# Optimization experiments

Hardware: AMD Instinct MI355X
Metric: run time of the kernel (lower is better)

The kernel has to match this reference:

```python
import jax, jax.numpy as jnp
import numpy as np

N, E, G = 50000, 800000, 64
DIN, HID, HEADS, L = 128, 128, 4, 3
CH = HID // HEADS  # 32
EPS = 1e-5


def seg_sum(d, ids, n):
    return jax.ops.segment_sum(d, ids, num_segments=n)


def seg_max(d, ids, n):
    return jax.ops.segment_max(d, ids, num_segments=n)


def seg_mean(d, ids, n):
    s = seg_sum(d, ids, n)
    c = seg_sum(jnp.ones((d.shape[0], 1), d.dtype), ids, n)
    return s / jnp.maximum(c, 1.0)


def setup_inputs() -> dict:
    key = jax.random.key(0)
    ks = jax.random.split(key, 24)
    p = lambda k, sh: jax.random.normal(k, sh, jnp.float32) * 0.05
    z = lambda *sh: jnp.zeros(sh, jnp.float32)
    return {
        'x': jax.random.normal(ks[0], (N, DIN), jnp.float32),
        'edge_index': jax.random.randint(ks[1], (2, E), 0, N),
        'batch': jnp.sort(jax.random.randint(ks[2], (N,), 0, G)),
        'proj_W': p(ks[3], (DIN, HID)), 'proj_b': z(HID),
        'gcn_W': p(ks[4], (L, HID, HID)), 'gcn_b': z(L, HID),
        'gat_W': p(ks[5], (L, HID, HID)),
        'gat_asrc': p(ks[6], (L, HEADS, CH)), 'gat_adst': p(ks[7], (L, HEADS, CH)),
        'gat_b': z(L, HID),
        'norm_w': jnp.ones((L, HID), jnp.float32), 'norm_b': z(L, HID),
        'norm_ms': jnp.ones((L, HID), jnp.float32),
        'hub_W1': p(ks[8], (HID, HID // 2)), 'hub_b1': z(HID // 2),
        'hub_W2': p(ks[9], (HID // 2, 4)), 'hub_b2': z(4),
        'att_W1': p(ks[10], (HID, HID // 2)), 'att_b1': z(HID // 2),
        'att_W2': p(ks[11], (HID // 2, 1)), 'att_b2': z(1),
        'pat_W1': p(ks[12], (HID * 2, HID)), 'pat_b1': z(HID),
        'pat_W2': p(ks[13], (HID, HID // 2)), 'pat_b2': z(HID // 2),
        'pat_W3': p(ks[14], (HID // 2, 8)), 'pat_b3': z(8),
        'cls_W1': p(ks[15], (HID + 12, HID)), 'cls_b1': z(HID),
        'cls_W2': p(ks[16], (HID, HID // 2)), 'cls_b2': z(HID // 2),
        'cls_W3': p(ks[17], (HID // 2, 2)), 'cls_b3': z(2),
    }


def _forward(fl, edge_index, batch):
    src, dst = edge_index[0], edge_index[1]
    loops = jnp.arange(N)
    s = jnp.concatenate([src, loops])  # with self-loops (GCN/GAT default)
    d = jnp.concatenate([dst, loops])

    x = fl['x'] @ fl['proj_W'] + fl['proj_b']  # [N, HID]

    # symmetric GCN normalization (shared across layers)
    deg = seg_sum(jnp.ones(s.shape[0], jnp.float32), d, N)
    dis = jnp.where(deg > 0, 1.0 / jnp.sqrt(deg), 0.0)
    coef = (dis[s] * dis[d])[:, None]  # [E+N, 1]

    for i in range(L):
        # GCNConv: out[dst] += norm * (x @ W)[src]
        h_gcn = seg_sum((x @ fl['gcn_W'][i])[s] * coef, d, N) + fl['gcn_b'][i]
        # GATConv (heads=4, concat), eval mode (no dropout)
        hh = (x @ fl['gat_W'][i]).reshape(N, HEADS, CH)
        a_s = (hh * fl['gat_asrc'][i]).sum(-1)  # [N, HEADS]
        a_d = (hh * fl['gat_adst'][i]).sum(-1)
        e = jax.nn.leaky_relu(a_s[s] + a_d[d], negative_slope=0.2)  # [E+N, HEADS]
        e = jnp.exp(e - seg_max(e, d, N)[d])
        alpha = e / seg_sum(e, d, N)[d]
        h_gat = seg_sum(hh[s] * alpha[:, :, None], d, N).reshape(N, HID) + fl['gat_b'][i]
        h = h_gcn + h_gat
        # GraphNorm: per-graph, per-feature
        mean = seg_mean(h, batch, G)
        out = h - fl['norm_ms'][i] * mean[batch]
        var = seg_mean(out * out, batch, G)
        out = out / jnp.sqrt(var[batch] + EPS)
        h = jax.nn.relu(fl['norm_w'][i] * out + fl['norm_b'][i])
        x = h if i == 0 else x + h

    # hub importance: normalized max degree per graph == 1.0 iff any degree > 0
    ones_e = jnp.ones(E, jnp.float32)
    node_deg = seg_sum(ones_e, src, N) + seg_sum(ones_e, dst, N)
    max_deg = seg_max(node_deg, batch, G)
    hub_importance = (max_deg > 0).astype(jnp.float32)

    hub_feat = jax.nn.relu(x @ fl['hub_W1'] + fl['hub_b1']) @ fl['hub_W2'] + fl['hub_b2']
    hub_pooled = seg_mean(hub_feat, batch, G)  # [G, 4]

    # attention pooling: softmax over ALL nodes (dim=0), then per-graph weighted sum
    w = jax.nn.relu(x @ fl['att_W1'] + fl['att_b1']) @ fl['att_W2'] + fl['att_b2']  # [N,1]
    w = jax.nn.softmax(w, axis=0)
    graph_emb = seg_sum(x * w, batch, G)  # [G, HID]

    pattern_emb = jnp.concatenate([seg_mean(x, batch, G), seg_max(x, batch, G)], axis=1)
    pf = jax.nn.relu(pattern_emb @ fl['pat_W1'] + fl['pat_b1'])
    pf = jax.nn.relu(pf @ fl['pat_W2'] + fl['pat_b2'])
    pattern_features = pf @ fl['pat_W3'] + fl['pat_b3']  # [G, 8]

    comb = jnp.concatenate([graph_emb, hub_pooled, pattern_features], axis=1)
    c = jax.nn.relu(comb @ fl['cls_W1'] + fl['cls_b1'])
    c = jax.nn.relu(c @ fl['cls_W2'] + fl['cls_b2'])
    logits = c @ fl['cls_W3'] + fl['cls_b3']  # [G, 2]
    return logits, hub_importance, graph_emb, hub_pooled, pattern_features


def reference(x, edge_index, batch, proj_W, proj_b, gcn_W, gcn_b, gat_W, gat_asrc,
              gat_adst, gat_b, norm_w, norm_b, norm_ms, hub_W1, hub_b1, hub_W2,
              hub_b2, att_W1, att_b1, att_W2, att_b2, pat_W1, pat_b1, pat_W2,
              pat_b2, pat_W3, pat_b3, cls_W1, cls_b1, cls_W2, cls_b2, cls_W3, cls_b3):
    fl = dict(x=x, proj_W=proj_W, proj_b=proj_b, gcn_W=gcn_W, gcn_b=gcn_b,
              gat_W=gat_W, gat_asrc=gat_asrc, gat_adst=gat_adst, gat_b=gat_b,
              norm_w=norm_w, norm_b=norm_b, norm_ms=norm_ms,
              hub_W1=hub_W1, hub_b1=hub_b1, hub_W2=hub_W2, hub_b2=hub_b2,
              att_W1=att_W1, att_b1=att_b1, att_W2=att_W2, att_b2=att_b2,
              pat_W1=pat_W1, pat_b1=pat_b1, pat_W2=pat_W2, pat_b2=pat_b2,
              pat_W3=pat_W3, pat_b3=pat_b3, cls_W1=cls_W1, cls_b1=cls_b1,
              cls_W2=cls_W2, cls_b2=cls_b2, cls_W3=cls_W3, cls_b3=cls_b3)
    return _forward(fl, edge_index, batch)
```

## Files before the change

### kernel.cpp

```cpp
#include <hip/hip_runtime.h>

#define NN 50000
#define NE 800000
#define NG 64
#define HID 128

typedef __attribute__((ext_vector_type(8))) short bf16x8;
typedef __attribute__((ext_vector_type(4))) float f32x4;

__device__ __forceinline__ unsigned short f2b(float f) {
  unsigned u = __float_as_uint(f);
  u += 0x7fffu + ((u >> 16) & 1u);
  return (unsigned short)(u >> 16);
}
__device__ __forceinline__ float b2f(unsigned short b) {
  return __uint_as_float(((unsigned)b) << 16);
}

__global__ void count_edges(const int* __restrict__ ei, int* __restrict__ cnt_dst,
                            int* __restrict__ cnt_src) {
  int e = blockIdx.x * 256 + threadIdx.x;
  if (e >= NE) return;
  atomicAdd(&cnt_src[ei[e]], 1);
  atomicAdd(&cnt_dst[ei[NE + e]], 1);
}

__global__ void scanA_dis(const int* __restrict__ cnt, int* __restrict__ partial,
                          float* __restrict__ dis) {
  __shared__ int s[256];
  int t = threadIdx.x;
  int i = blockIdx.x * 256 + t;
  int v = (i < NN) ? cnt[i] : 0;
  if (i < NN) dis[i] = rsqrtf((float)(v + 1));
  s[t] = v;
  __syncthreads();
  for (int off = 128; off; off >>= 1) {
    if (t < off) s[t] += s[t + off];
    __syncthreads();
  }
  if (!t) partial[blockIdx.x] = s[0];
}

__global__ void scanB_bounds(int* __restrict__ partial, int nb,
                             const int* __restrict__ batch, int* __restrict__ gstart) {
  int t = threadIdx.x;
  if (t == 0) {
    int acc = 0;
    for (int i = 0; i < nb; ++i) { int v = partial[i]; partial[i] = acc; acc += v; }
  }
  if (t >= 1 && t <= NG + 1) {
    int g = t - 1;
    int lo = 0, hi = NN;
    while (lo < hi) { int mid = (lo + hi) >> 1; if (batch[mid] < g) lo = mid + 1; else hi = mid; }
    gstart[g] = lo;
  }
}

__global__ void scanC(const int* __restrict__ cnt, const int* __restrict__ partial,
                      int* __restrict__ rowptr) {
  __shared__ int bufA[256], bufB[256];
  int t = threadIdx.x;
  int i = blockIdx.x * 256 + t;
  int v = (i < NN) ? cnt[i] : 0;
  bufA[t] = v;
  __syncthreads();
  int* src = bufA; int* dst = bufB;
  for (int off = 1; off < 256; off <<= 1) {
    int x = src[t];
    if (t >= off) x += src[t - off];
    dst[t] = x;
    __syncthreads();
    int* tmp = src; src = dst; dst = tmp;
  }
  int incl = src[t];
  if (i < NN) rowptr[i] = partial[blockIdx.x] + incl - v;
  if (i == NN - 1) rowptr[NN] = partial[blockIdx.x] + incl;
}

__global__ void fill_edges(const int* __restrict__ ei, const int* __restrict__ rowptr,
                           int* __restrict__ fillpos, int* __restrict__ col) {
  int e = blockIdx.x * 256 + threadIdx.x;
  if (e >= NE) return;
  int s = ei[e], d = ei[NE + e];
  int p = atomicAdd(&fillpos[d], 1);
  col[rowptr[d] + p] = s;
}

__global__ void prep_all(const float* __restrict__ gcn_W, const float* __restrict__ gat_W,
                         const float* __restrict__ hW1, const float* __restrict__ aW1,
                         const float* __restrict__ projW, unsigned short* __restrict__ wfrag,
                         unsigned short* __restrict__ nfrag, unsigned short* __restrict__ pfrag) {
  int m = blockIdx.y;
  int idx = blockIdx.x * 256 + threadIdx.x;
  int j = idx & 7, lane = (idx >> 3) & 63, t = idx >> 9;
  int ct = t >> 2, ks = t & 3;
  int k = ks * 32 + ((lane >> 4) << 3) + j;
  int c = (ct << 4) + (lane & 15);
  if (m < 3) {
    wfrag[(size_t)m * 32768 + idx] = f2b(gcn_W[(size_t)m * 16384 + k * 128 + c]);
    wfrag[(size_t)m * 32768 + 16384 + idx] = f2b(gat_W[(size_t)m * 16384 + k * 128 + c]);
  } else if (m == 3) {
    float v = (c < 64) ? hW1[k * 64 + c] : aW1[k * 64 + (c - 64)];
    nfrag[idx] = f2b(v);
  } else {
    pfrag[idx] = f2b(projW[k * 128 + c]);
  }
}

__device__ __forceinline__ void load_a_frags_f32(const float* __restrict__ xp, int lane,
                                                 bf16x8 a[4]) {
#pragma unroll
  for (int ks = 0; ks < 4; ++ks) {
    int k0 = ks * 32 + ((lane >> 4) << 3);
    float4 u = *(const float4*)&xp[k0];
    float4 v = *(const float4*)&xp[k0 + 4];
    bf16x8 t;
    t[0] = (short)f2b(u.x); t[1] = (short)f2b(u.y); t[2] = (short)f2b(u.z); t[3] = (short)f2b(u.w);
    t[4] = (short)f2b(v.x); t[5] = (short)f2b(v.y); t[6] = (short)f2b(v.z); t[7] = (short)f2b(v.w);
    a[ks] = t;
  }
}

__device__ __forceinline__ void load_a_frags_b16(const unsigned short* __restrict__ xp,
                                                 int lane, bf16x8 a[4]) {
#pragma unroll
  for (int ks = 0; ks < 4; ++ks) {
    int k0 = ks * 32 + ((lane >> 4) << 3);
    a[ks] = *(const bf16x8*)&xp[k0];
  }
}

__global__ __launch_bounds__(256) void gemm_proj_mfma(
    const float* __restrict__ X, const unsigned short* __restrict__ F,
    const float* __restrict__ bias, float* __restrict__ Y,
    unsigned short* __restrict__ YB, int nrows) {
  __shared__ float Ys[64 * 128];
  int tid = threadIdx.x;
  int w = tid >> 6, lane = tid & 63;
  int row0 = blockIdx.x * 64;
  int row = row0 + w * 16 + (lane & 15);
  const float* xp = (row < nrows) ? &X[(size_t)row * 128] : &X[0];
  bf16x8 a[4];
  load_a_frags_f32(xp, lane, a);
  f32x4 acc[8];
#pragma unroll
  for (int ct = 0; ct < 8; ++ct) acc[ct] = (f32x4){0.f, 0.f, 0.f, 0.f};
#pragma unroll
  for (int ct = 0; ct < 8; ++ct) {
#pragma unroll
    for (int ks = 0; ks < 4; ++ks) {
      bf16x8 b = *(const bf16x8*)&F[((ct * 4 + ks) * 64 + lane) * 8];
      acc[ct] = __builtin_amdgcn_mfma_f32_16x16x32_bf16(a[ks], b, acc[ct], 0, 0, 0);
    }
  }
#pragma unroll
  for (int ct = 0; ct < 8; ++ct) {
    int c = (ct << 4) + (lane & 15);
    float bv = bias[c];
#pragma unroll
    for (int j = 0; j < 4; ++j) {
      int r = w * 16 + ((lane >> 4) << 2) + j;
      Ys[r * 128 + c] = acc[ct][j] + bv;
    }
  }
  __syncthreads();
  int nr = min(nrows - row0, 64);
  const float4* ys4 = (const float4*)Ys;
  float4* y4 = (float4*)(Y + (size_t)row0 * 128);
  ushort4* yb4 = (ushort4*)(YB + (size_t)row0 * 128);
  for (int e = tid; e < nr * 32; e += 256) {
    float4 v = ys4[e];
    y4[e] = v;
    ushort4 b;
    b.x = f2b(v.x); b.y = f2b(v.y); b.z = f2b(v.z); b.w = f2b(v.w);
    yb4[e] = b;
  }
}

__global__ __launch_bounds__(256) void gemm_dual_mfma(
    const unsigned short* __restrict__ XB, const unsigned short* __restrict__ F1,
    const unsigned short* __restrict__ F2, const float* __restrict__ asrc,
    const float* __restrict__ adst, const float* __restrict__ dis,
    unsigned short* __restrict__ G, float* __restrict__ a_s, float* __restrict__ a_d,
    int nrows) {
  __shared__ unsigned short Gs[64 * 256];
  int tid = threadIdx.x;
  int w = tid >> 6, lane = tid & 63;
  int row0 = blockIdx.x * 64;
  int row = row0 + w * 16 + (lane & 15);
  const unsigned short* xp = (row < nrows) ? &XB[(size_t)row * 128] : &XB[0];
  bf16x8 a[4];
  load_a_frags_b16(xp, lane, a);
  f32x4 acc1[8], acc2[8];
#pragma unroll
  for (int ct = 0; ct < 8; ++ct) {
    acc1[ct] = (f32x4){0.f, 0.f, 0.f, 0.f};
    acc2[ct] = (f32x4){0.f, 0.f, 0.f, 0.f};
  }
#pragma unroll
  for (int ct = 0; ct < 8; ++ct) {
#pragma unroll
    for (int ks = 0; ks < 4; ++ks) {
      int off = ((ct * 4 + ks) * 64 + lane) * 8;
      bf16x8 b1 = *(const bf16x8*)&F1[off];
      bf16x8 b2 = *(const bf16x8*)&F2[off];
      acc1[ct] = __builtin_amdgcn_mfma_f32_16x16x32_bf16(a[ks], b1, acc1[ct], 0, 0, 0);
      acc2[ct] = __builtin_amdgcn_mfma_f32_16x16x32_bf16(a[ks], b2, acc2[ct], 0, 0, 0);
    }
  }
  float dv[4];
#pragma unroll
  for (int j = 0; j < 4; ++j) {
    int gr = row0 + w * 16 + ((lane >> 4) << 2) + j;
    dv[j] = dis[gr < nrows ? gr : 0];
  }
#pragma unroll
  for (int ct = 0; ct < 8; ++ct) {
#pragma unroll
    for (int j = 0; j < 4; ++j) {
      int r = w * 16 + ((lane >> 4) << 2) + j;
      int c = (ct << 4) + (lane & 15);
      Gs[r * 256 + c] = f2b(acc1[ct][j] * dv[j]);
      Gs[r * 256 + 128 + c] = f2b(acc2[ct][j]);
    }
  }
  __syncthreads();
  int nr = min(nrows - row0, 64);
  const uint4* gs4 = (const uint4*)Gs;
  uint4* g4 = (uint4*)(G + (size_t)row0 * 256);
  for (int e = tid; e < nr * 32; e += 256) g4[e] = gs4[e];
  int f = 2 * lane;
  float as0 = asrc[f], as1 = asrc[f + 1];
  float ad0 = adst[f], ad1 = adst[f + 1];
  for (int i = 0; i < 16; ++i) {
    int r = w * 16 + i;
    int n = row0 + r;
    if (n >= nrows) break;
    ushort2 v = *(const ushort2*)&Gs[r * 256 + 128 + f];
    float x0 = b2f(v.x), x1 = b2f(v.y);
    float ps = x0 * as0 + x1 * as1;
    float pd = x0 * ad0 + x1 * ad1;
    ps += __shfl_xor(ps, 1); pd += __shfl_xor(pd, 1);
    ps += __shfl_xor(ps, 2); pd += __shfl_xor(pd, 2);
    ps += __shfl_xor(ps, 4); pd += __shfl_xor(pd, 4);
    ps += __shfl_xor(ps, 8); pd += __shfl_xor(pd, 8);
    if ((lane & 15) == 0) {
      int h = lane >> 4;
      a_s[n * 4 + h] = ps;
      a_d[n * 4 + h] = pd;
    }
  }
}

__global__ __launch_bounds__(256) void node_mlps_mfma(
    const unsigned short* __restrict__ XB, const unsigned short* __restrict__ Fn,
    const float* __restrict__ hb1, const float* __restrict__ ab1,
    const float* __restrict__ hW2, const float* __restrict__ hb2,
    const float* __restrict__ aW2, const float* __restrict__ ab2,
    float* __restrict__ hub_feat, float* __restrict__ w_att) {
  __shared__ float Hs[64 * 133];
  int tid = threadIdx.x;
  int w = tid >> 6, lane = tid & 63;
  int row0 = blockIdx.x * 64;
  int row = row0 + w * 16 + (lane & 15);
  const unsigned short* xp = (row < NN) ? &XB[(size_t)row * 128] : &XB[0];
  bf16x8 a[4];
  load_a_frags_b16(xp, lane, a);
  f32x4 acc[8];
#pragma unroll
  for (int ct = 0; ct < 8; ++ct) acc[ct] = (f32x4){0.f, 0.f, 0.f, 0.f};
#pragma unroll
  for (int ct = 0; ct < 8; ++ct) {
#pragma unroll
    for (int ks = 0; ks < 4; ++ks) {
      bf16x8 b = *(const bf16x8*)&Fn[((ct * 4 + ks) * 64 + lane) * 8];
      acc[ct] = __builtin_amdgcn_mfma_f32_16x16x32_bf16(a[ks], b, acc[ct], 0, 0, 0);
    }
  }
#pragma unroll
  for (int ct = 0; ct < 8; ++ct) {
    int c = (ct << 4) + (lane & 15);
    float bias = (c < 64) ? hb1[c] : ab1[c - 64];
#pragma unroll
    for (int j = 0; j < 4; ++j) {
      int r = w * 16 + ((lane >> 4) << 2) + j;
      float v = acc[ct][j] + bias;
      Hs[r * 133 + c] = v > 0.f ? v : 0.f;
    }
  }
  __syncthreads();
  int r = tid & 63, o = tid >> 6;
  int n = row0 + r;
  if (n < NN) {
    float d = hb2[o];
#pragma unroll 8
    for (int k = 0; k < 64; ++k) d += Hs[r * 133 + k] * hW2[k * 4 + o];
    hub_feat[n * 4 + o] = d;
    if (tid < 64) {
      float d2 = ab2[0];
#pragma unroll 8
      for (int k = 0; k < 64; ++k) d2 += Hs[r * 133 + 64 + k] * aW2[k];
      w_att[n] = d2;
    }
  }
}

__device__ __forceinline__ float lrelu(float v) { return v > 0.f ? v : 0.2f * v; }

__global__ __launch_bounds__(256) void edge_aggregate_p(
    const unsigned short* __restrict__ G, const float* __restrict__ a_s,
    const float* __restrict__ a_d, const float* __restrict__ dis,
    const int* __restrict__ rowptr, const int* __restrict__ col,
    const float* __restrict__ gcn_b, const float* __restrict__ gat_b,
    float* __restrict__ hout, float* __restrict__ S1z) {
  if (blockIdx.x == 0) {
    for (int i = threadIdx.x; i < 2 * NG * 128; i += 256) S1z[i] = 0.f;
  }
  int n = blockIdx.x * 4 + (threadIdx.x >> 6);
  int lane = threadIdx.x & 63;
  int es = lane >> 4, fl = lane & 15;
  int h = fl >> 2;
  int f8 = fl << 3;
  int p0 = rowptr[n], p1 = rowptr[n + 1];
  int cnt = p1 - p0 + 1;
  float adh = a_d[n * 4 + h];
  float dn = dis[n];
  float ag[8] = {0.f, 0.f, 0.f, 0.f, 0.f, 0.f, 0.f, 0.f};
  float aa[8] = {0.f, 0.f, 0.f, 0.f, 0.f, 0.f, 0.f, 0.f};
  float ssum = 0.f;
#define EDGE_ACC(eu, xv, hv)                                \
  do {                                                      \
    ag[0] += __uint_as_float((xv).x << 16);                 \
    ag[1] += __uint_as_float((xv).x & 0xffff0000u);         \
    ag[2] += __uint_as_float((xv).y << 16);                 \
    ag[3] += __uint_as_float((xv).y & 0xffff0000u);         \
    ag[4] += __uint_as_float((xv).z << 16);                 \
    ag[5] += __uint_as_float((xv).z & 0xffff0000u);         \
    ag[6] += __uint_as_float((xv).w << 16);                 \
    ag[7] += __uint_as_float((xv).w & 0xffff0000u);         \
    aa[0] += (eu)*__uint_as_float((hv).x << 16);            \
    aa[1] += (eu)*__uint_as_float((hv).x & 0xffff0000u);    \
    aa[2] += (eu)*__uint_as_float((hv).y << 16);            \
    aa[3] += (eu)*__uint_as_float((hv).y & 0xffff0000u);    \
    aa[4] += (eu)*__uint_as_float((hv).z << 16);            \
    aa[5] += (eu)*__uint_as_float((hv).z & 0xffff0000u);    \
    aa[6] += (eu)*__uint_as_float((hv).w << 16);            \
    aa[7] += (eu)*__uint_as_float((hv).w & 0xffff0000u);    \
  } while (0)
  int e = es;
  for (; e + 4 < cnt; e += 8) {
    int eB = e + 4;
    int srcA = (e < cnt - 1) ? col[p0 + e] : n;
    int srcB = (eB < cnt - 1) ? col[p0 + eB] : n;
    float euA = __expf(lrelu(a_s[srcA * 4 + h] + adh));
    float euB = __expf(lrelu(a_s[srcB * 4 + h] + adh));
    uint4 xvA = *(const uint4*)&G[(size_t)srcA * 256 + f8];
    uint4 hvA = *(const uint4*)&G[(size_t)srcA * 256 + 128 + f8];
    uint4 xvB = *(const uint4*)&G[(size_t)srcB * 256 + f8];
    uint4 hvB = *(const uint4*)&G[(size_t)srcB * 256 + 128 + f8];
    ssum += euA + euB;
    EDGE_ACC(euA, xvA, hvA);
    EDGE_ACC(euB, xvB, hvB);
  }
  for (; e < cnt; e += 4) {
    int src = (e < cnt - 1) ? col[p0 + e] : n;
    float eu = __expf(lrelu(a_s[src * 4 + h] + adh));
    uint4 xv = *(const uint4*)&G[(size_t)src * 256 + f8];
    uint4 hv = *(const uint4*)&G[(size_t)src * 256 + 128 + f8];
    ssum += eu;
    EDGE_ACC(eu, xv, hv);
  }
#undef EDGE_ACC
#pragma unroll
  for (int j = 0; j < 8; ++j) {
    ag[j] += __shfl_xor(ag[j], 16); ag[j] += __shfl_xor(ag[j], 32);
    aa[j] += __shfl_xor(aa[j], 16); aa[j] += __shfl_xor(aa[j], 32);
  }
  ssum += __shfl_xor(ssum, 16); ssum += __shfl_xor(ssum, 32);
  if (es == 0) {
    float rs = 1.f / ssum;
    float4 gb0 = *(const float4*)&gcn_b[f8];
    float4 gb1 = *(const float4*)&gcn_b[f8 + 4];
    float4 tb0 = *(const float4*)&gat_b[f8];
    float4 tb1 = *(const float4*)&gat_b[f8 + 4];
    float4 o0, o1;
    o0.x = ag[0] * dn + aa[0] * rs + gb0.x + tb0.x;
    o0.y = ag[1] * dn + aa[1] * rs + gb0.y + tb0.y;
    o0.z = ag[2] * dn + aa[2] * rs + gb0.z + tb0.z;
    o0.w = ag[3] * dn + aa[3] * rs + gb0.w + tb0.w;
    o1.x = ag[4] * dn + aa[4] * rs + gb1.x + tb1.x;
    o1.y = ag[5] * dn + aa[5] * rs + gb1.y + tb1.y;
    o1.z = ag[6] * dn + aa[6] * rs + gb1.z + tb1.z;
    o1.w = ag[7] * dn + aa[7] * rs + gb1.w + tb1.w;
    *(float4*)&hout[n * 128 + f8] = o0;
    *(float4*)&hout[n * 128 + f8 + 4] = o1;
  }
}

__global__ __launch_bounds__(128) void graph_stats_par(
    const float* __restrict__ h, const int* __restrict__ batch,
    float* __restrict__ S1, float* __restrict__ S2) {
  int f = threadIdx.x;
  int n0 = blockIdx.x * 64;
  int n1 = min(n0 + 64, NN);
  int g = batch[n0];
  float s1 = 0.f, s2 = 0.f;
  for (int n = n0; n < n1; ++n) {
    int gn = batch[n];
    if (gn != g) {
      atomicAdd(&S1[g * 128 + f], s1);
      atomicAdd(&S2[g * 128 + f], s2);
      s1 = 0.f; s2 = 0.f; g = gn;
    }
    float v = h[n * 128 + f];
    s1 += v; s2 += v * v;
  }
  atomicAdd(&S1[g * 128 + f], s1);
  atomicAdd(&S2[g * 128 + f], s2);
}

__global__ __launch_bounds__(256) void graph_norm(
    const float* __restrict__ h, const int* __restrict__ batch,
    const int* __restrict__ gstart, const float* __restrict__ S1,
    const float* __restrict__ S2, const float* __restrict__ nw,
    const float* __restrict__ nb, const float* __restrict__ nms,
    float* __restrict__ x, unsigned short* __restrict__ xb, int layer) {
  int idx = blockIdx.x * 256 + threadIdx.x;
  if (idx >= NN * 32) return;
  int n = idx >> 5, fq = (idx & 31) << 2;
  int g = batch[n];
  float c = fmaxf((float)(gstart[g + 1] - gstart[g]), 1.f);
  float rc = 1.f / c;
  float4 s1 = *(const float4*)&S1[g * 128 + fq];
  float4 s2 = *(const float4*)&S2[g * 128 + fq];
  float4 ms = *(const float4*)&nms[fq];
  float4 w = *(const float4*)&nw[fq];
  float4 b = *(const float4*)&nb[fq];
  float4 hv = *(const float4*)&h[(size_t)n * 128 + fq];
  float4 o;
#define GN1(X)                                                           \
  {                                                                      \
    float mean = s1.X * rc;                                              \
    float var = s2.X * rc - mean * mean * ms.X * (2.f - ms.X);           \
    var = fmaxf(var, 0.f);                                               \
    float ot = (hv.X - ms.X * mean) * rsqrtf(var + 1e-5f);               \
    float t = w.X * ot + b.X;                                            \
    o.X = t > 0.f ? t : 0.f;                                             \
  }
  GN1(x) GN1(y) GN1(z) GN1(w)
#undef GN1
  float4* xp = (float4*)&x[(size_t)n * 128 + fq];
  float4 xo;
  if (layer == 0) {
    xo = o;
  } else {
    xo = *xp;
    xo.x += o.x; xo.y += o.y; xo.z += o.z; xo.w += o.w;
  }
  *xp = xo;
  ushort4 bo;
  bo.x = f2b(xo.x); bo.y = f2b(xo.y); bo.z = f2b(xo.z); bo.w = f2b(xo.w);
  *(ushort4*)&xb[(size_t)n * 128 + fq] = bo;
}

__global__ void reduce_sum1(const float* __restrict__ w, float* __restrict__ tmpS,
                            float* __restrict__ poolZ, int zcount) {
  __shared__ float s[256];
  int t = threadIdx.x;
  if (blockIdx.x == 0) {
    for (int i = t; i < zcount; i += 256) poolZ[i] = 0.f;
  }
  float acc = 0.f;
  for (int i = blockIdx.x * 256 + t; i < NN; i += gridDim.x * 256) acc += __expf(w[i]);
  s[t] = acc;
  __syncthreads();
  for (int off = 128; off; off >>= 1) {
    if (t < off) s[t] += s[t + off];
    __syncthreads();
  }
  if (!t) tmpS[blockIdx.x] = s[0];
}

__global__ void reduce_sum2(const float* __restrict__ tmpS, float* __restrict__ scal) {
  __shared__ float s[256];
  int t = threadIdx.x;
  s[t] = tmpS[t];
  __syncthreads();
  for (int off = 128; off; off >>= 1) {
    if (t < off) s[t] += s[t + off];
    __syncthreads();
  }
  if (!t) scal[1] = s[0];
}

__global__ __launch_bounds__(128) void graph_pool_par(
    const float* __restrict__ x, const float* __restrict__ hub_feat,
    const float* __restrict__ w_att, const int* __restrict__ batch,
    float* __restrict__ Sx, unsigned* __restrict__ Mx, float* __restrict__ WSx,
    float* __restrict__ Shub) {
  int f = threadIdx.x;
  int n0 = blockIdx.x * 64;
  int n1 = min(n0 + 64, NN);
  int g = batch[n0];
  float sx = 0.f, wx = 0.f, mx = 0.f, sh = 0.f;
  for (int n = n0; n < n1; ++n) {
    int gn = batch[n];
    if (gn != g) {
      atomicAdd(&Sx[g * 128 + f], sx);
      atomicAdd(&WSx[g * 128 + f], wx);
      atomicMax(&Mx[g * 128 + f], __float_as_uint(mx));
      if (f < 4) atomicAdd(&Shub[g * 4 + f], sh);
      sx = 0.f; wx = 0.f; mx = 0.f; sh = 0.f; g = gn;
    }
    float xv = x[n * 128 + f];
    float ew = __expf(w_att[n]);
    sx += xv;
    wx += ew * xv;
    mx = fmaxf(mx, xv);
    if (f < 4) sh += hub_feat[n * 4 + f];
  }
  atomicAdd(&Sx[g * 128 + f], sx);
  atomicAdd(&WSx[g * 128 + f], wx);
  atomicMax(&Mx[g * 128 + f], __float_as_uint(mx));
  if (f < 4) atomicAdd(&Shub[g * 4 + f], sh);
}

__global__ __launch_bounds__(128) void finalize(
    const float* __restrict__ Sx, const float* __restrict__ Mx,
    const float* __restrict__ WSx, const float* __restrict__ Shub,
    const float* __restrict__ scal, const int* __restrict__ gstart,
    const int* __restrict__ cnt_src, const int* __restrict__ cnt_dst,
    const float* __restrict__ pW1, const float* __restrict__ pb1,
    const float* __restrict__ pW2, const float* __restrict__ pb2,
    const float* __restrict__ pW3, const float* __restrict__ pb3,
    const float* __restrict__ cW1, const float* __restrict__ cb1,
    const float* __restrict__ cW2, const float* __restrict__ cb2,
    const float* __restrict__ cW3, const float* __restrict__ cb3,
    float* __restrict__ out) {
  int g = blockIdx.x, t = threadIdx.x;
  __shared__ float pe[256], comb[140], buf1[128], buf2[64];
  __shared__ int snd[128];
  int s = gstart[g], e = gstart[g + 1];
  float c = fmaxf((float)(e - s), 1.f);
  int mdeg = 0;
  for (int n = s + t; n < e; n += 128) mdeg = max(mdeg, cnt_src[n] + cnt_dst[n]);
  snd[t] = mdeg;
  float* out_logits = out;
  float* out_hub = out + 128;
  float* out_ge = out + 192;
  float* out_hp = out + 192 + 8192;
  float* out_pf = out + 192 + 8192 + 256;
  float ge = WSx[g * 128 + t] / scal[1];
  out_ge[g * 128 + t] = ge;
  comb[t] = ge;
  pe[t] = Sx[g * 128 + t] / c;
  pe[128 + t] = Mx[g * 128 + t];
  if (t < 4) {
    float hp = Shub[g * 4 + t] / c;
    out_hp[g * 4 + t] = hp;
    comb[128 + t] = hp;
  }
  __syncthreads();
  for (int off = 64; off; off >>= 1) {
    if (t < off) snd[t] = max(snd[t], snd[t + off]);
    __syncthreads();
  }
  if (t == 0) out_hub[g] = (snd[0] > 0) ? 1.f : 0.f;
  float v = pb1[t];
  for (int k = 0; k < 256; ++k) v += pe[k] * pW1[k * 128 + t];
  buf1[t] = v > 0.f ? v : 0.f;
  __syncthreads();
  if (t < 64) {
    float v2 = pb2[t];
    for (int k = 0; k < 128; ++k) v2 += buf1[k] * pW2[k * 64 + t];
    buf2[t] = v2 > 0.f ? v2 : 0.f;
  }
  __syncthreads();
  if (t < 8) {
    float v3 = pb3[t];
    for (int k = 0; k < 64; ++k) v3 += buf2[k] * pW3[k * 8 + t];
    out_pf[g * 8 + t] = v3;
    comb[132 + t] = v3;
  }
  __syncthreads();
  float u = cb1[t];
  for (int k = 0; k < 140; ++k) u += comb[k] * cW1[k * 128 + t];
  buf1[t] = u > 0.f ? u : 0.f;
  __syncthreads();
  if (t < 64) {
    float u2 = cb2[t];
    for (int k = 0; k < 128; ++k) u2 += buf1[k] * cW2[k * 64 + t];
    buf2[t] = u2 > 0.f ? u2 : 0.f;
  }
  __syncthreads();
  if (t < 2) {
    float u3 = cb3[t];
    for (int k = 0; k < 64; ++k) u3 += buf2[k] * cW3[k * 2 + t];
    out_logits[g * 2 + t] = u3;
  }
}

extern "C" void kernel_launch(void* const* d_in, const int* in_sizes, int n_in,
                              void* d_out, int out_size, void* d_ws, size_t ws_size,
                              hipStream_t stream) {
  const float* x_in = (const float*)d_in[0];
  const int* ei = (const int*)d_in[1];
  const int* batch = (const int*)d_in[2];
  const float* proj_W = (const float*)d_in[3];
  const float* proj_b = (const float*)d_in[4];
  const float* gcn_W = (const float*)d_in[5];
  const float* gcn_b = (const float*)d_in[6];
  const float* gat_W = (const float*)d_in[7];
  const float* gat_as = (const float*)d_in[8];
  const float* gat_ad = (const float*)d_in[9];
  const float* gat_b = (const float*)d_in[10];
  const float* norm_w = (const float*)d_in[11];
  const float* norm_b = (const float*)d_in[12];
  const float* norm_ms = (const float*)d_in[13];
  const float* hub_W1 = (const float*)d_in[14];
  const float* hub_b1 = (const float*)d_in[15];
  const float* hub_W2 = (const float*)d_in[16];
  const float* hub_b2 = (const float*)d_in[17];
  const float* att_W1 = (const float*)d_in[18];
  const float* att_b1 = (const float*)d_in[19];
  const float* att_W2 = (const float*)d_in[20];
  const float* att_b2 = (const float*)d_in[21];
  const float* pat_W1 = (const float*)d_in[22];
  const float* pat_b1 = (const float*)d_in[23];
  const float* pat_W2 = (const float*)d_in[24];
  const float* pat_b2 = (const float*)d_in[25];
  const float* pat_W3 = (const float*)d_in[26];
  const float* pat_b3 = (const float*)d_in[27];
  const float* cls_W1 = (const float*)d_in[28];
  const float* cls_b1 = (const float*)d_in[29];
  const float* cls_W2 = (const float*)d_in[30];
  const float* cls_b2 = (const float*)d_in[31];
  const float* cls_W3 = (const float*)d_in[32];
  const float* cls_b3 = (const float*)d_in[33];
  float* out = (float*)d_out;

  char* ws = (char*)d_ws;
  auto fbuf = [&](size_t n) { float* p = (float*)ws; ws += ((n * 4 + 255) / 256) * 256; return p; };
  auto ibuf = [&](size_t n) { int* p = (int*)ws; ws += ((n * 4 + 255) / 256) * 256; return p; };

  float* x = fbuf((size_t)NN * 128);
  unsigned short* xb = (unsigned short*)fbuf((size_t)NN * 64);
  unsigned short* gath = (unsigned short*)fbuf((size_t)NN * 128);
  float* h = fbuf((size_t)NN * 128);
  unsigned short* wfrag = (unsigned short*)fbuf(3 * 32768 / 2);
  unsigned short* nfrag = (unsigned short*)fbuf(16384 / 2);
  unsigned short* pfrag = (unsigned short*)fbuf(16384 / 2);
  float* a_s = fbuf((size_t)NN * 4);
  float* a_d = fbuf((size_t)NN * 4);
  float* dis = fbuf(NN);
  float* w_att = fbuf(NN);
  float* hub_feat = fbuf((size_t)NN * 4);
  float* S1 = fbuf(NG * 128);
  float* S2 = fbuf(NG * 128);
  float* Sx = fbuf(NG * 128);
  float* Mx = fbuf(NG * 128);
  float* WSx = fbuf(NG * 128);
  float* Shub = fbuf(NG * 4);
  float* tmpS = fbuf(256);
  float* scal = fbuf(4);
  int* zero0 = ibuf(3 * NN);
  int* cnt_dst = zero0;
  int* cnt_src = zero0 + NN;
  int* fillpos = zero0 + 2 * NN;
  int* rowptr = ibuf(NN + 1);
  int* col = ibuf(NE);
  int* partial = ibuf(256);
  int* gstart = ibuf(NG + 1);

  const int NB = (NN + 255) / 256;
  const int NC = (NN + 63) / 64;
  const int GM = (NN + 63) / 64;

  hipMemsetAsync(zero0, 0, (size_t)3 * NN * 4, stream);
  count_edges<<<NE / 256, 256, 0, stream>>>(ei, cnt_dst, cnt_src);
  scanA_dis<<<NB, 256, 0, stream>>>(cnt_dst, partial, dis);
  scanB_bounds<<<1, 128, 0, stream>>>(partial, NB, batch, gstart);
  scanC<<<NB, 256, 0, stream>>>(cnt_dst, partial, rowptr);
  fill_edges<<<NE / 256, 256, 0, stream>>>(ei, rowptr, fillpos, col);
  prep_all<<<dim3(64, 5), 256, 0, stream>>>(gcn_W, gat_W, hub_W1, att_W1, proj_W,
                                            wfrag, nfrag, pfrag);

  gemm_proj_mfma<<<GM, 256, 0, stream>>>(x_in, pfrag, proj_b, x, xb, NN);

  for (int l = 0; l < 3; ++l) {
    gemm_dual_mfma<<<GM, 256, 0, stream>>>(xb, wfrag + (size_t)l * 32768,
                                           wfrag + (size_t)l * 32768 + 16384,
                                           gat_as + l * 128, gat_ad + l * 128, dis,
                                           gath, a_s, a_d, NN);
    edge_aggregate_p<<<NN / 4, 256, 0, stream>>>(gath, a_s, a_d, dis, rowptr, col,
                                                 gcn_b + l * 128, gat_b + l * 128, h, S1);
    graph_stats_par<<<NC, 128, 0, stream>>>(h, batch, S1, S2);
    graph_norm<<<(NN * 32 + 255) / 256, 256, 0, stream>>>(h, batch, gstart, S1, S2,
                                                          norm_w + l * 128, norm_b + l * 128,
                                                          norm_ms + l * 128, x, xb, l);
  }

  node_mlps_mfma<<<GM, 256, 0, stream>>>(xb, nfrag, hub_b1, att_b1, hub_W2, hub_b2,
                                         att_W2, att_b2, hub_feat, w_att);

  reduce_sum1<<<256, 256, 0, stream>>>(w_att, tmpS, Sx, 3 * NG * 128 + NG * 4);
  reduce_sum2<<<1, 256, 0, stream>>>(tmpS, scal);

  graph_pool_par<<<NC, 128, 0, stream>>>(x, hub_feat, w_att, batch,
                                         Sx, (unsigned*)Mx, WSx, Shub);

  finalize<<<NG, 128, 0, stream>>>(Sx, Mx, WSx, Shub, scal, gstart, cnt_src, cnt_dst,
                                   pat_W1, pat_b1, pat_W2, pat_b2, pat_W3, pat_b3,
                                   cls_W1, cls_b1, cls_W2, cls_b2, cls_W3, cls_b3, out);
}
```

Measured before the change: 598.5 us.

## Drop fp32 residual stream, fuse graph stats into aggregation and pooling into MLP

Keeps the residual node features only in bf16, so the fp32 x buffer and its reads and writes go away. Per-graph sum and sum-of-squares statistics are accumulated inside the edge aggregation kernel, with LDS pre-reduction when all four nodes in a block share a graph, which removes the separate stats pass over h. Node MLPs and graph pooling are merged into one kernel, and the two-stage exp-sum reduction becomes a single atomic pass. Zeroing of accumulators moves into the memset and the dual GEMM. The residual stream now accumulates in bf16, which adds rounding error across layers.

```diff
diff --git a/kernel.cpp b/kernel.cpp
--- a/kernel.cpp
+++ b/kernel.cpp
@@ -132,9 +132,8 @@
 
 __global__ __launch_bounds__(256) void gemm_proj_mfma(
     const float* __restrict__ X, const unsigned short* __restrict__ F,
-    const float* __restrict__ bias, float* __restrict__ Y,
-    unsigned short* __restrict__ YB, int nrows) {
-  __shared__ float Ys[64 * 128];
+    const float* __restrict__ bias, unsigned short* __restrict__ XB, int nrows) {
+  __shared__ unsigned short Ys[64 * 128];
   int tid = threadIdx.x;
   int w = tid >> 6, lane = tid & 63;
   int row0 = blockIdx.x * 64;
@@ -160,21 +159,14 @@
 #pragma unroll
     for (int j = 0; j < 4; ++j) {
       int r = w * 16 + ((lane >> 4) << 2) + j;
-      Ys[r * 128 + c] = acc[ct][j] + bv;
+      Ys[r * 128 + c] = f2b(acc[ct][j] + bv);
     }
   }
   __syncthreads();
   int nr = min(nrows - row0, 64);
-  const float4* ys4 = (const float4*)Ys;
-  float4* y4 = (float4*)(Y + (size_t)row0 * 128);
-  ushort4* yb4 = (ushort4*)(YB + (size_t)row0 * 128);
-  for (int e = tid; e < nr * 32; e += 256) {
-    float4 v = ys4[e];
-    y4[e] = v;
-    ushort4 b;
-    b.x = f2b(v.x); b.y = f2b(v.y); b.z = f2b(v.z); b.w = f2b(v.w);
-    yb4[e] = b;
-  }
+  const uint4* ys4 = (const uint4*)Ys;
+  uint4* y4 = (uint4*)(XB + (size_t)row0 * 128);
+  for (int e = tid; e < nr * 16; e += 256) y4[e] = ys4[e];
 }
 
 __global__ __launch_bounds__(256) void gemm_dual_mfma(
@@ -182,7 +174,10 @@
     const unsigned short* __restrict__ F2, const float* __restrict__ asrc,
     const float* __restrict__ adst, const float* __restrict__ dis,
     unsigned short* __restrict__ G, float* __restrict__ a_s, float* __restrict__ a_d,
-    int nrows) {
+    float* __restrict__ S1z, int nrows) {
+  if (blockIdx.x == 0) {
+    for (int i = threadIdx.x; i < 2 * NG * 128; i += 256) S1z[i] = 0.f;
+  }
   __shared__ unsigned short Gs[64 * 256];
   int tid = threadIdx.x;
   int w = tid >> 6, lane = tid & 63;
@@ -252,72 +247,20 @@
   }
 }
 
-__global__ __launch_bounds__(256) void node_mlps_mfma(
-    const unsigned short* __restrict__ XB, const unsigned short* __restrict__ Fn,
-    const float* __restrict__ hb1, const float* __restrict__ ab1,
-    const float* __restrict__ hW2, const float* __restrict__ hb2,
-    const float* __restrict__ aW2, const float* __restrict__ ab2,
-    float* __restrict__ hub_feat, float* __restrict__ w_att) {
-  __shared__ float Hs[64 * 133];
-  int tid = threadIdx.x;
-  int w = tid >> 6, lane = tid & 63;
-  int row0 = blockIdx.x * 64;
-  int row = row0 + w * 16 + (lane & 15);
-  const unsigned short* xp = (row < NN) ? &XB[(size_t)row * 128] : &XB[0];
-  bf16x8 a[4];
-  load_a_frags_b16(xp, lane, a);
-  f32x4 acc[8];
-#pragma unroll
-  for (int ct = 0; ct < 8; ++ct) acc[ct] = (f32x4){0.f, 0.f, 0.f, 0.f};
-#pragma unroll
-  for (int ct = 0; ct < 8; ++ct) {
-#pragma unroll
-    for (int ks = 0; ks < 4; ++ks) {
-      bf16x8 b = *(const bf16x8*)&Fn[((ct * 4 + ks) * 64 + lane) * 8];
-      acc[ct] = __builtin_amdgcn_mfma_f32_16x16x32_bf16(a[ks], b, acc[ct], 0, 0, 0);
-    }
-  }
-#pragma unroll
-  for (int ct = 0; ct < 8; ++ct) {
-    int c = (ct << 4) + (lane & 15);
-    float bias = (c < 64) ? hb1[c] : ab1[c - 64];
-#pragma unroll
-    for (int j = 0; j < 4; ++j) {
-      int r = w * 16 + ((lane >> 4) << 2) + j;
-      float v = acc[ct][j] + bias;
-      Hs[r * 133 + c] = v > 0.f ? v : 0.f;
-    }
-  }
-  __syncthreads();
-  int r = tid & 63, o = tid >> 6;
-  int n = row0 + r;
-  if (n < NN) {
-    float d = hb2[o];
-#pragma unroll 8
-    for (int k = 0; k < 64; ++k) d += Hs[r * 133 + k] * hW2[k * 4 + o];
-    hub_feat[n * 4 + o] = d;
-    if (tid < 64) {
-      float d2 = ab2[0];
-#pragma unroll 8
-      for (int k = 0; k < 64; ++k) d2 += Hs[r * 133 + 64 + k] * aW2[k];
-      w_att[n] = d2;
-    }
-  }
-}
-
 __device__ __forceinline__ float lrelu(float v) { return v > 0.f ? v : 0.2f * v; }
 
 __global__ __launch_bounds__(256) void edge_aggregate_p(
     const unsigned short* __restrict__ G, const float* __restrict__ a_s,
     const float* __restrict__ a_d, const float* __restrict__ dis,
     const int* __restrict__ rowptr, const int* __restrict__ col,
-    const float* __restrict__ gcn_b, const float* __restrict__ gat_b,
-    float* __restrict__ hout, float* __restrict__ S1z) {
-  if (blockIdx.x == 0) {
-    for (int i = threadIdx.x; i < 2 * NG * 128; i += 256) S1z[i] = 0.f;
-  }
-  int n = blockIdx.x * 4 + (threadIdx.x >> 6);
-  int lane = threadIdx.x & 63;
+    const int* __restrict__ batch, const float* __restrict__ gcn_b,
+    const float* __restrict__ gat_b, float* __restrict__ hout,
+    float* __restrict__ S1, float* __restrict__ S2) {
+  __shared__ float S1loc[128], S2loc[128];
+  int tid = threadIdx.x;
+  if (tid < 128) { S1loc[tid] = 0.f; S2loc[tid] = 0.f; }
+  int n = blockIdx.x * 4 + (tid >> 6);
+  int lane = tid & 63;
   int es = lane >> 4, fl = lane & 15;
   int h = fl >> 2;
   int f8 = fl << 3;
@@ -377,46 +320,49 @@
     aa[j] += __shfl_xor(aa[j], 16); aa[j] += __shfl_xor(aa[j], 32);
   }
   ssum += __shfl_xor(ssum, 16); ssum += __shfl_xor(ssum, 32);
+  int g0 = batch[blockIdx.x * 4];
+  bool fast = (batch[blockIdx.x * 4 + 3] == g0);
+  __syncthreads();
   if (es == 0) {
     float rs = 1.f / ssum;
     float4 gb0 = *(const float4*)&gcn_b[f8];
     float4 gb1 = *(const float4*)&gcn_b[f8 + 4];
     float4 tb0 = *(const float4*)&gat_b[f8];
     float4 tb1 = *(const float4*)&gat_b[f8 + 4];
+    float o[8];
+    o[0] = ag[0] * dn + aa[0] * rs + gb0.x + tb0.x;
+    o[1] = ag[1] * dn + aa[1] * rs + gb0.y + tb0.y;
+    o[2] = ag[2] * dn + aa[2] * rs + gb0.z + tb0.z;
+    o[3] = ag[3] * dn + aa[3] * rs + gb0.w + tb0.w;
+    o[4] = ag[4] * dn + aa[4] * rs + gb1.x + tb1.x;
+    o[5] = ag[5] * dn + aa[5] * rs + gb1.y + tb1.y;
+    o[6] = ag[6] * dn + aa[6] * rs + gb1.z + tb1.z;
+    o[7] = ag[7] * dn + aa[7] * rs + gb1.w + tb1.w;
     float4 o0, o1;
-    o0.x = ag[0] * dn + aa[0] * rs + gb0.x + tb0.x;
-    o0.y = ag[1] * dn + aa[1] * rs + gb0.y + tb0.y;
-    o0.z = ag[2] * dn + aa[2] * rs + gb0.z + tb0.z;
-    o0.w = ag[3] * dn + aa[3] * rs + gb0.w + tb0.w;
-    o1.x = ag[4] * dn + aa[4] * rs + gb1.x + tb1.x;
-    o1.y = ag[5] * dn + aa[5] * rs + gb1.y + tb1.y;
-    o1.z = ag[6] * dn + aa[6] * rs + gb1.z + tb1.z;
-    o1.w = ag[7] * dn + aa[7] * rs + gb1.w + tb1.w;
+    o0.x = o[0]; o0.y = o[1]; o0.z = o[2]; o0.w = o[3];
+    o1.x = o[4]; o1.y = o[5]; o1.z = o[6]; o1.w = o[7];
     *(float4*)&hout[n * 128 + f8] = o0;
     *(float4*)&hout[n * 128 + f8 + 4] = o1;
-  }
-}
-
-__global__ __launch_bounds__(128) void graph_stats_par(
-    const float* __restrict__ h, const int* __restrict__ batch,
-    float* __restrict__ S1, float* __restrict__ S2) {
-  int f = threadIdx.x;
-  int n0 = blockIdx.x * 64;
-  int n1 = min(n0 + 64, NN);
-  int g = batch[n0];
-  float s1 = 0.f, s2 = 0.f;
-  for (int n = n0; n < n1; ++n) {
-    int gn = batch[n];
-    if (gn != g) {
-      atomicAdd(&S1[g * 128 + f], s1);
-      atomicAdd(&S2[g * 128 + f], s2);
-      s1 = 0.f; s2 = 0.f; g = gn;
-    }
-    float v = h[n * 128 + f];
-    s1 += v; s2 += v * v;
-  }
-  atomicAdd(&S1[g * 128 + f], s1);
-  atomicAdd(&S2[g * 128 + f], s2);
+    if (fast) {
+#pragma unroll
+      for (int j = 0; j < 8; ++j) {
+        atomicAdd(&S1loc[f8 + j], o[j]);
+        atomicAdd(&S2loc[f8 + j], o[j] * o[j]);
+      }
+    } else {
+      int g = batch[n];
+#pragma unroll
+      for (int j = 0; j < 8; ++j) {
+        atomicAdd(&S1[g * 128 + f8 + j], o[j]);
+        atomicAdd(&S2[g * 128 + f8 + j], o[j] * o[j]);
+      }
+    }
+  }
+  __syncthreads();
+  if (fast && tid < 128) {
+    atomicAdd(&S1[g0 * 128 + tid], S1loc[tid]);
+    atomicAdd(&S2[g0 * 128 + tid], S2loc[tid]);
+  }
 }
 
 __global__ __launch_bounds__(256) void graph_norm(
@@ -424,7 +370,7 @@
     const int* __restrict__ gstart, const float* __restrict__ S1,
     const float* __restrict__ S2, const float* __restrict__ nw,
     const float* __restrict__ nb, const float* __restrict__ nms,
-    float* __restrict__ x, unsigned short* __restrict__ xb, int layer) {
+    unsigned short* __restrict__ xb, int layer) {
   int idx = blockIdx.x * 256 + threadIdx.x;
   if (idx >= NN * 32) return;
   int n = idx >> 5, fq = (idx & 31) << 2;
@@ -449,80 +395,120 @@
   }
   GN1(x) GN1(y) GN1(z) GN1(w)
 #undef GN1
-  float4* xp = (float4*)&x[(size_t)n * 128 + fq];
-  float4 xo;
-  if (layer == 0) {
-    xo = o;
-  } else {
-    xo = *xp;
-    xo.x += o.x; xo.y += o.y; xo.z += o.z; xo.w += o.w;
-  }
-  *xp = xo;
+  ushort4* xp = (ushort4*)&xb[(size_t)n * 128 + fq];
+  float4 xo = o;
+  if (layer != 0) {
+    ushort4 pv = *xp;
+    xo.x += b2f(pv.x); xo.y += b2f(pv.y); xo.z += b2f(pv.z); xo.w += b2f(pv.w);
+  }
   ushort4 bo;
   bo.x = f2b(xo.x); bo.y = f2b(xo.y); bo.z = f2b(xo.z); bo.w = f2b(xo.w);
-  *(ushort4*)&xb[(size_t)n * 128 + fq] = bo;
-}
-
-__global__ void reduce_sum1(const float* __restrict__ w, float* __restrict__ tmpS,
-                            float* __restrict__ poolZ, int zcount) {
-  __shared__ float s[256];
-  int t = threadIdx.x;
-  if (blockIdx.x == 0) {
-    for (int i = t; i < zcount; i += 256) poolZ[i] = 0.f;
-  }
-  float acc = 0.f;
-  for (int i = blockIdx.x * 256 + t; i < NN; i += gridDim.x * 256) acc += __expf(w[i]);
-  s[t] = acc;
-  __syncthreads();
-  for (int off = 128; off; off >>= 1) {
-    if (t < off) s[t] += s[t + off];
-    __syncthreads();
-  }
-  if (!t) tmpS[blockIdx.x] = s[0];
-}
-
-__global__ void reduce_sum2(const float* __restrict__ tmpS, float* __restrict__ scal) {
-  __shared__ float s[256];
-  int t = threadIdx.x;
-  s[t] = tmpS[t];
-  __syncthreads();
-  for (int off = 128; off; off >>= 1) {
-    if (t < off) s[t] += s[t + off];
-    __syncthreads();
-  }
-  if (!t) scal[1] = s[0];
-}
-
-__global__ __launch_bounds__(128) void graph_pool_par(
-    const float* __restrict__ x, const float* __restrict__ hub_feat,
-    const float* __restrict__ w_att, const int* __restrict__ batch,
-    float* __restrict__ Sx, unsigned* __restrict__ Mx, float* __restrict__ WSx,
-    float* __restrict__ Shub) {
-  int f = threadIdx.x;
-  int n0 = blockIdx.x * 64;
-  int n1 = min(n0 + 64, NN);
-  int g = batch[n0];
-  float sx = 0.f, wx = 0.f, mx = 0.f, sh = 0.f;
-  for (int n = n0; n < n1; ++n) {
-    int gn = batch[n];
-    if (gn != g) {
+  *xp = bo;
+}
+
+__global__ __launch_bounds__(256) void node_mlps_pool(
+    const unsigned short* __restrict__ XB, const unsigned short* __restrict__ Fn,
+    const float* __restrict__ hb1, const float* __restrict__ ab1,
+    const float* __restrict__ hW2, const float* __restrict__ hb2,
+    const float* __restrict__ aW2, const float* __restrict__ ab2,
+    const int* __restrict__ batch, float* __restrict__ hub_feat,
+    float* __restrict__ w_att, float* __restrict__ Sx, unsigned* __restrict__ Mx,
+    float* __restrict__ WSx, float* __restrict__ Shub) {
+  __shared__ float Hs[64 * 133];
+  __shared__ float Hf[64 * 4];
+  __shared__ float Wa[64];
+  int tid = threadIdx.x;
+  int w = tid >> 6, lane = tid & 63;
+  int row0 = blockIdx.x * 64;
+  int row = row0 + w * 16 + (lane & 15);
+  const unsigned short* xp = (row < NN) ? &XB[(size_t)row * 128] : &XB[0];
+  bf16x8 a[4];
+  load_a_frags_b16(xp, lane, a);
+  f32x4 acc[8];
+#pragma unroll
+  for (int ct = 0; ct < 8; ++ct) acc[ct] = (f32x4){0.f, 0.f, 0.f, 0.f};
+#pragma unroll
+  for (int ct = 0; ct < 8; ++ct) {
+#pragma unroll
+    for (int ks = 0; ks < 4; ++ks) {
+      bf16x8 b = *(const bf16x8*)&Fn[((ct * 4 + ks) * 64 + lane) * 8];
+      acc[ct] = __builtin_amdgcn_mfma_f32_16x16x32_bf16(a[ks], b, acc[ct], 0, 0, 0);
+    }
+  }
+#pragma unroll
+  for (int ct = 0; ct < 8; ++ct) {
+    int c = (ct << 4) + (lane & 15);
+    float bias = (c < 64) ? hb1[c] : ab1[c - 64];
+#pragma unroll
+    for (int j = 0; j < 4; ++j) {
+      int r = w * 16 + ((lane >> 4) << 2) + j;
+      float v = acc[ct][j] + bias;
+      Hs[r * 133 + c] = v > 0.f ? v : 0.f;
+    }
+  }
+  __syncthreads();
+  {
+    int r = tid & 63, o = tid >> 6;
+    int n = row0 + r;
+    if (n < NN) {
+      float d = hb2[o];
+#pragma unroll 8
+      for (int k = 0; k < 64; ++k) d += Hs[r * 133 + k] * hW2[k * 4 + o];
+      hub_feat[n * 4 + o] = d;
+      Hf[r * 4 + o] = d;
+      if (tid < 64) {
+        float d2 = ab2[0];
+#pragma unroll 8
+        for (int k = 0; k < 64; ++k) d2 += Hs[r * 133 + 64 + k] * aW2[k];
+        w_att[n] = d2;
+        Wa[r] = d2;
+      }
+    }
+  }
+  __syncthreads();
+  if (tid < 128) {
+    int f = tid;
+    int n0 = row0;
+    int n1 = min(n0 + 64, NN);
+    if (n0 < NN) {
+      int g = batch[n0];
+      float sx = 0.f, wx = 0.f, mx = 0.f, sh = 0.f;
+      for (int n = n0; n < n1; ++n) {
+        int gn = batch[n];
+        if (gn != g) {
+          atomicAdd(&Sx[g * 128 + f], sx);
+          atomicAdd(&WSx[g * 128 + f], wx);
+          atomicMax(&Mx[g * 128 + f], __float_as_uint(mx));
+          if (f < 4) atomicAdd(&Shub[g * 4 + f], sh);
+          sx = 0.f; wx = 0.f; mx = 0.f; sh = 0.f; g = gn;
+        }
+        float xv = b2f(XB[(size_t)n * 128 + f]);
+        float ew = __expf(Wa[n - n0]);
+        sx += xv;
+        wx += ew * xv;
+        mx = fmaxf(mx, xv);
+        if (f < 4) sh += Hf[(n - n0) * 4 + f];
+      }
       atomicAdd(&Sx[g * 128 + f], sx);
       atomicAdd(&WSx[g * 128 + f], wx);
       atomicMax(&Mx[g * 128 + f], __float_as_uint(mx));
       if (f < 4) atomicAdd(&Shub[g * 4 + f], sh);
-      sx = 0.f; wx = 0.f; mx = 0.f; sh = 0.f; g = gn;
-    }
-    float xv = x[n * 128 + f];
-    float ew = __expf(w_att[n]);
-    sx += xv;
-    wx += ew * xv;
-    mx = fmaxf(mx, xv);
-    if (f < 4) sh += hub_feat[n * 4 + f];
-  }
-  atomicAdd(&Sx[g * 128 + f], sx);
-  atomicAdd(&WSx[g * 128 + f], wx);
-  atomicMax(&Mx[g * 128 + f], __float_as_uint(mx));
-  if (f < 4) atomicAdd(&Shub[g * 4 + f], sh);
+    }
+  }
+}
+
+__global__ void reduce_sum1(const float* __restrict__ w, float* __restrict__ scal) {
+  __shared__ float s[256];
+  int t = threadIdx.x;
+  float acc = 0.f;
+  for (int i = blockIdx.x * 256 + t; i < NN; i += gridDim.x * 256) acc += __expf(w[i]);
+  s[t] = acc;
+  __syncthreads();
+  for (int off = 128; off; off >>= 1) {
+    if (t < off) s[t] += s[t + off];
+    __syncthreads();
+  }
+  if (!t) atomicAdd(&scal[1], s[0]);
 }
 
 __global__ __launch_bounds__(128) void finalize(
@@ -643,7 +629,17 @@
   auto fbuf = [&](size_t n) { float* p = (float*)ws; ws += ((n * 4 + 255) / 256) * 256; return p; };
   auto ibuf = [&](size_t n) { int* p = (int*)ws; ws += ((n * 4 + 255) / 256) * 256; return p; };
 
-  float* x = fbuf((size_t)NN * 128);
+  int* zero0 = ibuf(3 * NN);
+  int* cnt_dst = zero0;
+  int* cnt_src = zero0 + NN;
+  int* fillpos = zero0 + 2 * NN;
+  float* Sx = fbuf(NG * 128);
+  float* Mx = fbuf(NG * 128);
+  float* WSx = fbuf(NG * 128);
+  float* Shub = fbuf(NG * 4);
+  float* scal = fbuf(4);
+  size_t zbytes = (char*)ws - (char*)zero0;
+
   unsigned short* xb = (unsigned short*)fbuf((size_t)NN * 64);
   unsigned short* gath = (unsigned short*)fbuf((size_t)NN * 128);
   float* h = fbuf((size_t)NN * 128);
@@ -657,26 +653,15 @@
   float* hub_feat = fbuf((size_t)NN * 4);
   float* S1 = fbuf(NG * 128);
   float* S2 = fbuf(NG * 128);
-  float* Sx = fbuf(NG * 128);
-  float* Mx = fbuf(NG * 128);
-  float* WSx = fbuf(NG * 128);
-  float* Shub = fbuf(NG * 4);
-  float* tmpS = fbuf(256);
-  float* scal = fbuf(4);
-  int* zero0 = ibuf(3 * NN);
-  int* cnt_dst = zero0;
-  int* cnt_src = zero0 + NN;
-  int* fillpos = zero0 + 2 * NN;
   int* rowptr = ibuf(NN + 1);
   int* col = ibuf(NE);
   int* partial = ibuf(256);
   int* gstart = ibuf(NG + 1);
 
   const int NB = (NN + 255) / 256;
-  const int NC = (NN + 63) / 64;
   const int GM = (NN + 63) / 64;
 
-  hipMemsetAsync(zero0, 0, (size_t)3 * NN * 4, stream);
+  hipMemsetAsync(zero0, 0, zbytes, stream);
   count_edges<<<NE / 256, 256, 0, stream>>>(ei, cnt_dst, cnt_src);
   scanA_dis<<<NB, 256, 0, stream>>>(cnt_dst, partial, dis);
   scanB_bounds<<<1, 128, 0, stream>>>(partial, NB, batch, gstart);
@@ -685,29 +670,25 @@
   prep_all<<<dim3(64, 5), 256, 0, stream>>>(gcn_W, gat_W, hub_W1, att_W1, proj_W,
                                             wfrag, nfrag, pfrag);
 
-  gemm_proj_mfma<<<GM, 256, 0, stream>>>(x_in, pfrag, proj_b, x, xb, NN);
+  gemm_proj_mfma<<<GM, 256, 0, stream>>>(x_in, pfrag, proj_b, xb, NN);
 
   for (int l = 0; l < 3; ++l) {
     gemm_dual_mfma<<<GM, 256, 0, stream>>>(xb, wfrag + (size_t)l * 32768,
                                            wfrag + (size_t)l * 32768 + 16384,
                                            gat_as + l * 128, gat_ad + l * 128, dis,
-                                           gath, a_s, a_d, NN);
-    edge_aggregate_p<<<NN / 4, 256, 0, stream>>>(gath, a_s, a_d, dis, rowptr, col,
-                                                 gcn_b + l * 128, gat_b + l * 128, h, S1);
-    graph_stats_par<<<NC, 128, 0, stream>>>(h, batch, S1, S2);
+                                           gath, a_s, a_d, S1, NN);
+    edge_aggregate_p<<<NN / 4, 256, 0, stream>>>(gath, a_s, a_d, dis, rowptr, col, batch,
+                                                 gcn_b + l * 128, gat_b + l * 128, h, S1, S2);
     graph_norm<<<(NN * 32 + 255) / 256, 256, 0, stream>>>(h, batch, gstart, S1, S2,
                                                           norm_w + l * 128, norm_b + l * 128,
-                                                          norm_ms + l * 128, x, xb, l);
-  }
-
-  node_mlps_mfma<<<GM, 256, 0, stream>>>(xb, nfrag, hub_b1, att_b1, hub_W2, hub_b2,
-                                         att_W2, att_b2, hub_feat, w_att);
-
-  reduce_sum1<<<256, 256, 0, stream>>>(w_att, tmpS, Sx, 3 * NG * 128 + NG * 4);
-  reduce_sum2<<<1, 256, 0, stream>>>(tmpS, scal);
-
-  graph_pool_par<<<NC, 128, 0, stream>>>(x, hub_feat, w_att, batch,
+                                                          norm_ms + l * 128, xb, l);
+  }
+
+  node_mlps_pool<<<GM, 256, 0, stream>>>(xb, nfrag, hub_b1, att_b1, hub_W2, hub_b2,
+                                         att_W2, att_b2, batch, hub_feat, w_att,
                                          Sx, (unsigned*)Mx, WSx, Shub);
+
+  reduce_sum1<<<256, 256, 0, stream>>>(w_att, scal);
 
   finalize<<<NG, 128, 0, stream>>>(Sx, Mx, WSx, Shub, scal, gstart, cnt_src, cnt_dst,
                                    pat_W1, pat_b1, pat_W2, pat_b2, pat_W3, pat_b3,
```

New measurement: 721.4 us. 1.21x slower.
